# Kernel tuning notes

Hardware: AMD Instinct MI355X
Metric: run time of the kernel (lower is better)

Reference implementation:

```python
import jax, jax.numpy as jnp
import numpy as np

B, S, HID, NH = 8, 384, 512, 8
HD = HID // NH
SCALE = float(np.sqrt(HID))  # torch code scales by sqrt(full hidden_units), not head dim
EPS = 1e-6


def setup_inputs() -> dict:
    key = jax.random.key(0)
    ks = jax.random.split(key, 6)
    enc = jax.random.normal(ks[0], (B, S, HID), jnp.float32)
    # mask: (B,1,S,S); fill=ones, made causal (lower-triangular) so masking is exercised
    mask = jnp.broadcast_to(jnp.tril(jnp.ones((S, S), jnp.int32)), (B, 1, S, S))
    init = 1.0 / np.sqrt(HID)
    Wq = jax.random.normal(ks[1], (HID, HID), jnp.float32) * init
    Wk = jax.random.normal(ks[2], (HID, HID), jnp.float32) * init
    Wv = jax.random.normal(ks[3], (HID, HID), jnp.float32) * init
    Wo = jax.random.normal(ks[4], (HID, HID), jnp.float32) * init
    ln_gamma = jnp.ones((HID,), jnp.float32)
    ln_beta = jnp.zeros((HID,), jnp.float32)
    return {"enc": enc, "mask": mask, "Wq": Wq, "Wk": Wk, "Wv": Wv, "Wo": Wo,
            "ln_gamma": ln_gamma, "ln_beta": ln_beta}


def reference(enc, mask, Wq, Wk, Wv, Wo, ln_gamma, ln_beta):
    # enc: (B,S,HID); torch Linear(no bias): y = x @ W.T
    def heads(x, W):
        return (x @ W.T).reshape(B, S, NH, HD).transpose(0, 2, 1, 3)  # (B,H,S,D)

    q, k, v = heads(enc, Wq), heads(enc, Wk), heads(enc, Wv)
    # intersample scores: query (b,h,q) vs key (c,h,k) -> (B,H,C,Sq,Sk)
    scores = jnp.einsum('bhqd,chkd->bhcqk', q, k) / SCALE
    m = mask[:, 0]  # (C,S,S): key-sample mask
    scores = jnp.where(m[None, None] == 0, -1.0e9, scores)
    # joint softmax over (key-sample c, key-position k)
    sw = scores.transpose(0, 1, 3, 2, 4).reshape(B, NH, S, B * S)
    w = jax.nn.softmax(sw, axis=-1).reshape(B, NH, S, B, S).transpose(0, 1, 3, 2, 4)  # (B,H,C,Sq,Sk)
    ctx = jnp.einsum('bhcqk,chkd->bhqd', w, v)            # (B,H,S,D)
    ctx = ctx.transpose(0, 2, 1, 3).reshape(B, S, HID)     # (B,S,HID)
    out = ctx @ Wo.T + enc                                 # W_O + residual (dropout=identity, eval)
    mu = out.mean(-1, keepdims=True)
    var = ((out - mu) ** 2).mean(-1, keepdims=True)
    out = (out - mu) / jnp.sqrt(var + EPS) * ln_gamma + ln_beta
    return (out, w)
```

## Files before the change

### kernel.cpp

```cpp
#include <hip/hip_runtime.h>
#include <hip/hip_cooperative_groups.h>
#include <hip/hip_bf16.h>

namespace cg = cooperative_groups;

#define B_    8
#define S_    384
#define HID_  512
#define NH_   8
#define HD_   64
#define T_    3072
static constexpr float INV_SCALE = 0.044194173824159216f;

typedef float  f32x4  __attribute__((ext_vector_type(4)));
typedef __bf16 bf16x8 __attribute__((ext_vector_type(8)));
typedef __bf16 bf16x4 __attribute__((ext_vector_type(4)));

#define MFMA(a, b, c) __builtin_amdgcn_mfma_f32_16x16x32_bf16((a), (b), (c), 0, 0, 0)

#define NTHR 512
#define SMEM_BYTES 22528


__device__ __forceinline__ void cvt_unit(int i,
    const float* __restrict__ enc, const float* __restrict__ Wq,
    const float* __restrict__ Wk,  const float* __restrict__ Wv,
    const float* __restrict__ Wo,
    __bf16* __restrict__ encB, __bf16* __restrict__ WqB,
    __bf16* __restrict__ WkB,  __bf16* __restrict__ WvB,
    __bf16* __restrict__ WoB)
{
    const int E  = T_ * HID_ / 4;
    const int W4 = HID_ * HID_ / 4;
    const float* src; __bf16* dst; int off;
    if      (i < E)          { src = enc; dst = encB; off = i; }
    else if (i < E + W4)     { src = Wq;  dst = WqB;  off = i - E; }
    else if (i < E + 2 * W4) { src = Wk;  dst = WkB;  off = i - E - W4; }
    else if (i < E + 3 * W4) { src = Wv;  dst = WvB;  off = i - E - 2 * W4; }
    else                     { src = Wo;  dst = WoB;  off = i - E - 3 * W4; }
    f32x4 v = *(const f32x4*)(src + (size_t)off * 4);
    bf16x4 o;
    #pragma unroll
    for (int j = 0; j < 4; ++j) o[j] = (__bf16)v[j];
    *(bf16x4*)(dst + (size_t)off * 4) = o;
}

__device__ __forceinline__ void qkv_unit(int vb, int t2,
    const __bf16* __restrict__ encB, const __bf16* __restrict__ WqB,
    const __bf16* __restrict__ WkB,  const __bf16* __restrict__ WvB,
    __bf16* __restrict__ Qs, __bf16* __restrict__ Ks, __bf16* __restrict__ Vt)
{
    const int w    = t2 >> 6;
    const int lane = t2 & 63;
    const int col  = lane & 15;
    const int quad = lane >> 4;
    const int x  = vb % 48;
    const int y  = (vb / 48) % 8;
    const int z  = vb / 384;
    const int m0 = x * 64 + w * 16;
    const int n0 = y * 64;
    const __bf16* W = (z == 0) ? WqB : (z == 1) ? WkB : WvB;

    f32x4 acc[4];
    #pragma unroll
    for (int j = 0; j < 4; ++j) acc[j] = (f32x4){0.f, 0.f, 0.f, 0.f};

    const __bf16* arow = encB + (size_t)(m0 + col) * HID_;
    for (int k0 = 0; k0 < HID_; k0 += 32) {
        bf16x8 a = *(const bf16x8*)(arow + k0 + quad * 8);
        #pragma unroll
        for (int j = 0; j < 4; ++j) {
            bf16x8 b = *(const bf16x8*)(W + (size_t)(n0 + j * 16 + col) * HID_ + k0 + quad * 8);
            acc[j] = MFMA(a, b, acc[j]);
        }
    }

    if (z == 2) {
        #pragma unroll
        for (int j = 0; j < 4; ++j) {
            int n = n0 + j * 16 + col;
            bf16x4 pk;
            #pragma unroll
            for (int r = 0; r < 4; ++r) pk[r] = (__bf16)acc[j][r];
            *(bf16x4*)(Vt + (size_t)n * T_ + m0 + quad * 4) = pk;
        }
    } else {
        __bf16* Oo = (z == 0) ? Qs : Ks;
        float sc = (z == 0) ? INV_SCALE : 1.0f;
        #pragma unroll
        for (int j = 0; j < 4; ++j)
            #pragma unroll
            for (int r = 0; r < 4; ++r)
                Oo[(size_t)(m0 + quad * 4 + r) * HID_ + n0 + j * 16 + col] =
                    (__bf16)(acc[j][r] * sc);
    }
}

__device__ __forceinline__ void attn_unit(int qt, int h, int b, int tid, char* smem,
    const __bf16* __restrict__ Qs, const __bf16* __restrict__ Ks,
    const __bf16* __restrict__ Vt, __bf16* __restrict__ ctxB,
    float* __restrict__ rlws, __bf16* __restrict__ eB,
    float* __restrict__ wout, int useBf16)
{
    const int W    = tid >> 6;
    const int half = W >> 2;
    const int w    = W & 3;
    const int lane = tid & 63;
    const int col  = lane & 15;
    const int quad = lane >> 4;

    __bf16 (*elds)[16][72] = (__bf16(*)[16][72])(smem);
    float  (*cred)[16][68] = (float(*)[16][68])(smem);
    float  (*lred)[16][16] = (float(*)[16][16])(smem + 18432);

    const int qq_base = w * 16 + quad * 4;

    const __bf16* qrow = Qs + (size_t)(b * S_ + qt * 64 + w * 16 + col) * HID_ + h * HD_;
    bf16x8 aQ0 = *(const bf16x8*)(qrow + quad * 8);
    bf16x8 aQ1 = *(const bf16x8*)(qrow + 32 + quad * 8);

    f32x4 acc[4];
    #pragma unroll
    for (int j = 0; j < 4; ++j) acc[j] = (f32x4){0.f, 0.f, 0.f, 0.f};
    float lp[4] = {0.f, 0.f, 0.f, 0.f};

    const size_t qg   = (size_t)(b * NH_ + h) * S_ + qt * 64 + w * 16 + col;
    __bf16* ebase = eB + qg * T_;
    float*  wbase = wout + (((size_t)(b * NH_ + h) * B_) * S_ + qt * 64 + w * 16 + col) * S_;

    const int NC = B_ * (qt + 1);
    for (int idx = half; idx < NC; idx += 2) {
        const int c  = idx / (qt + 1);
        const int kc = idx % (qt + 1);
        const int kt0 = c * S_ + kc * 64;
        const bool diag = (kc == qt);
        #pragma unroll
        for (int nt = 0; nt < 4; ++nt) {
            const __bf16* krow = Ks + (size_t)(kt0 + nt * 16 + col) * HID_ + h * HD_;
            bf16x8 bK0 = *(const bf16x8*)(krow + quad * 8);
            bf16x8 bK1 = *(const bf16x8*)(krow + 32 + quad * 8);
            f32x4 s = (f32x4){0.f, 0.f, 0.f, 0.f};
            s = MFMA(aQ0, bK0, s);
            s = MFMA(aQ1, bK1, s);
            const int kk = nt * 16 + col;
            #pragma unroll
            for (int r = 0; r < 4; ++r) {
                float e = (!diag || kk <= qq_base + r) ? __expf(s[r]) : 0.f;
                lp[r] += e;
                elds[W][quad * 4 + r][kk] = (__bf16)e;
            }
        }
        #pragma unroll
        for (int ks = 0; ks < 2; ++ks) {
            bf16x8 aE = *(const bf16x8*)(&elds[W][col][ks * 32 + quad * 8]);
            if (useBf16) {
                *(bf16x8*)(ebase + c * S_ + kc * 64 + ks * 32 + quad * 8) = aE;
            } else {
                float* wp = wbase + (size_t)c * S_ * S_ + kc * 64 + ks * 32 + quad * 8;
                f32x4 lo, hi;
                #pragma unroll
                for (int j = 0; j < 4; ++j) { lo[j] = (float)aE[j]; hi[j] = (float)aE[j + 4]; }
                *(f32x4*)wp = lo;
                *(f32x4*)(wp + 4) = hi;
            }
            #pragma unroll
            for (int nt = 0; nt < 4; ++nt) {
                bf16x8 bV = *(const bf16x8*)(Vt + (size_t)(h * HD_ + nt * 16 + col) * T_ +
                                             kt0 + ks * 32 + quad * 8);
                acc[nt] = MFMA(aE, bV, acc[nt]);
            }
        }
    }

    __syncthreads();

    if (half == 1) {
        #pragma unroll
        for (int nt = 0; nt < 4; ++nt)
            #pragma unroll
            for (int r = 0; r < 4; ++r)
                cred[w][quad * 4 + r][nt * 16 + col] = acc[nt][r];
        #pragma unroll
        for (int r = 0; r < 4; ++r)
            lred[w][quad * 4 + r][col] = lp[r];
    }
    __syncthreads();
    if (half == 0) {
        #pragma unroll
        for (int r = 0; r < 4; ++r)
            lp[r] += lred[w][quad * 4 + r][col];
        #pragma unroll
        for (int nt = 0; nt < 4; ++nt)
            #pragma unroll
            for (int r = 0; r < 4; ++r)
                acc[nt][r] += cred[w][quad * 4 + r][nt * 16 + col];

        float rl[4];
        #pragma unroll
        for (int r = 0; r < 4; ++r) {
            float v = lp[r];
            v += __shfl_xor(v, 1);
            v += __shfl_xor(v, 2);
            v += __shfl_xor(v, 4);
            v += __shfl_xor(v, 8);
            rl[r] = 1.0f / v;
        }
        if (col == 0) {
            #pragma unroll
            for (int r = 0; r < 4; ++r)
                rlws[(size_t)(b * NH_ + h) * S_ + qt * 64 + qq_base + r] = rl[r];
        }
        #pragma unroll
        for (int nt = 0; nt < 4; ++nt)
            #pragma unroll
            for (int r = 0; r < 4; ++r)
                ctxB[(size_t)(b * S_ + qt * 64 + qq_base + r) * HID_ + h * HD_ + nt * 16 + col] =
                    (__bf16)(acc[nt][r] * rl[r]);
    }
}

__device__ __forceinline__ void wscale_unit(int u2, int tid, int nthr,
    const float* __restrict__ rlws, const __bf16* __restrict__ eB,
    float* __restrict__ wout, int useBf16)
{
    const int bh = u2 >> 3;
    const int c  = u2 & 7;
    float* wbase = wout + ((size_t)bh * B_ + c) * S_ * S_;
    const __bf16* ebase = eB + (size_t)bh * S_ * T_ + c * S_;
    const float* rlbase = rlws + (size_t)bh * S_;

    const int NCHUNK = S_ * (S_ / 8);
    for (int idx = tid; idx < NCHUNK; idx += nthr) {
        const int q  = idx / 48;
        const int k8 = (idx - q * 48) * 8;
        float* wp = wbase + (size_t)q * S_ + k8;
        if ((k8 >> 6) > (q >> 6)) {
            *(f32x4*)wp       = (f32x4){0.f, 0.f, 0.f, 0.f};
            *(f32x4*)(wp + 4) = (f32x4){0.f, 0.f, 0.f, 0.f};
        } else {
            const float rl = rlbase[q];
            f32x4 lo, hi;
            if (useBf16) {
                bf16x8 e = *(const bf16x8*)(ebase + (size_t)q * T_ + k8);
                #pragma unroll
                for (int j = 0; j < 4; ++j) { lo[j] = (float)e[j] * rl; hi[j] = (float)e[j + 4] * rl; }
            } else {
                f32x4 e0 = *(const f32x4*)wp;
                f32x4 e1 = *(const f32x4*)(wp + 4);
                #pragma unroll
                for (int j = 0; j < 4; ++j) { lo[j] = e0[j] * rl; hi[j] = e1[j] * rl; }
            }
            *(f32x4*)wp       = lo;
            *(f32x4*)(wp + 4) = hi;
        }
    }
}

__global__ __launch_bounds__(512, 2)
void mega2(const float* __restrict__ enc,
           const float* __restrict__ Wq,  const float* __restrict__ Wk,
           const float* __restrict__ Wv,  const float* __restrict__ Wo,
           const float* __restrict__ gamma, const float* __restrict__ beta,
           __bf16* __restrict__ encB, __bf16* __restrict__ WqB,
           __bf16* __restrict__ WkB,  __bf16* __restrict__ WvB,
           __bf16* __restrict__ WoB,
           __bf16* __restrict__ Qs,   __bf16* __restrict__ Ks,
           __bf16* __restrict__ Vt,   __bf16* __restrict__ ctxB,
           float* __restrict__ rlws,  __bf16* __restrict__ eB,
           float* __restrict__ wout,  float* __restrict__ out, int useBf16)
{
    cg::grid_group grid = cg::this_grid();
    const int blk  = blockIdx.x;
    const int nblk = gridDim.x;
    const int tid  = threadIdx.x;

    __shared__ __align__(16) char smem[SMEM_BYTES];

    {
        const int TOT = T_ * HID_ / 4 + HID_ * HID_;
        for (int i = blk * NTHR + tid; i < TOT; i += nblk * NTHR)
            cvt_unit(i, enc, Wq, Wk, Wv, Wo, encB, WqB, WkB, WvB, WoB);
    }
    grid.sync();

    {
        const int half = tid >> 8;
        const int t2   = tid & 255;
        for (int u = blk; u < 576; u += nblk)
            qkv_unit(u * 2 + half, t2, encB, WqB, WkB, WvB, Qs, Ks, Vt);
    }
    grid.sync();

    for (int i = blk; i < 384; i += nblk) {
        const int qt = 5 - (i >> 6);
        const int r  = i & 63;
        attn_unit(qt, r & 7, r >> 3, tid, smem, Qs, Ks, Vt, ctxB, rlws, eB, wout, useBf16);
        __syncthreads();
    }
    grid.sync();

    for (int u = blk; u < 704; u += nblk) {
        if (u < 192) {
            const int t0   = u * 16;
            const int wv   = tid >> 6;
            const int lane = tid & 63;
            const int col  = lane & 15;
            const int quad = lane >> 4;
            float (*s_sums)[8][2] = (float(*)[8][2])(smem);

            f32x4 acc[4];
            #pragma unroll
            for (int nt = 0; nt < 4; ++nt) acc[nt] = (f32x4){0.f, 0.f, 0.f, 0.f};

            const __bf16* arow = ctxB + (size_t)(t0 + col) * HID_;
            for (int step = 0; step < 16; ++step) {
                bf16x8 a = *(const bf16x8*)(arow + step * 32 + quad * 8);
                #pragma unroll
                for (int nt = 0; nt < 4; ++nt) {
                    bf16x8 bW = *(const bf16x8*)(WoB + (size_t)(wv * 64 + nt * 16 + col) * HID_ +
                                                 step * 32 + quad * 8);
                    acc[nt] = MFMA(a, bW, acc[nt]);
                }
            }

            const int trow = t0 + quad * 4;
            float psum[4] = {0.f, 0.f, 0.f, 0.f};
            float psq[4]  = {0.f, 0.f, 0.f, 0.f};
            #pragma unroll
            for (int nt = 0; nt < 4; ++nt) {
                int n = wv * 64 + nt * 16 + col;
                #pragma unroll
                for (int r = 0; r < 4; ++r) {
                    float x = acc[nt][r] + enc[(size_t)(trow + r) * HID_ + n];
                    acc[nt][r] = x;
                    psum[r] += x;
                    psq[r]  += x * x;
                }
            }
            #pragma unroll
            for (int r = 0; r < 4; ++r) {
                float v = psum[r], q2 = psq[r];
                v  += __shfl_xor(v, 1);  v  += __shfl_xor(v, 2);
                v  += __shfl_xor(v, 4);  v  += __shfl_xor(v, 8);
                q2 += __shfl_xor(q2, 1); q2 += __shfl_xor(q2, 2);
                q2 += __shfl_xor(q2, 4); q2 += __shfl_xor(q2, 8);
                if (col == 0) {
                    s_sums[quad * 4 + r][wv][0] = v;
                    s_sums[quad * 4 + r][wv][1] = q2;
                }
            }
            __syncthreads();

            #pragma unroll
            for (int r = 0; r < 4; ++r) {
                float sm = 0.f, sq = 0.f;
                #pragma unroll
                for (int q = 0; q < 8; ++q) {
                    sm += s_sums[quad * 4 + r][q][0];
                    sq += s_sums[quad * 4 + r][q][1];
                }
                float mu   = sm * (1.0f / 512.0f);
                float var  = sq * (1.0f / 512.0f) - mu * mu;
                float rstd = rsqrtf(var + 1e-6f);
                #pragma unroll
                for (int nt = 0; nt < 4; ++nt) {
                    int n = wv * 64 + nt * 16 + col;
                    float y = (acc[nt][r] - mu) * rstd * gamma[n] + beta[n];
                    out[(size_t)(trow + r) * HID_ + n] = y;
                }
            }
            __syncthreads();
        } else {
            wscale_unit(u - 192, tid, NTHR, rlws, eB, wout, useBf16);
        }
    }
}

__global__ __launch_bounds__(256)
void cvt_kernel(const float* enc, const float* Wq, const float* Wk,
                const float* Wv, const float* Wo,
                __bf16* encB, __bf16* WqB, __bf16* WkB, __bf16* WvB, __bf16* WoB)
{
    int i = blockIdx.x * 256 + threadIdx.x;
    cvt_unit(i, enc, Wq, Wk, Wv, Wo, encB, WqB, WkB, WvB, WoB);
}

__global__ __launch_bounds__(256)
void qkv_kernel(const __bf16* encB, const __bf16* WqB, const __bf16* WkB,
                const __bf16* WvB, __bf16* Qs, __bf16* Ks, __bf16* Vt)
{
    int vb = blockIdx.x + 48 * (blockIdx.y + 8 * blockIdx.z);
    qkv_unit(vb, threadIdx.x, encB, WqB, WkB, WvB, Qs, Ks, Vt);
}

__global__ __launch_bounds__(512)
void attn_sep(const __bf16* Qs, const __bf16* Ks, const __bf16* Vt,
              __bf16* ctxB, float* rlws, __bf16* eB, float* wout, int useBf16)
{
    __shared__ __align__(16) char smem[SMEM_BYTES];
    const int i  = blockIdx.x;
    const int qt = 5 - (i >> 6);
    const int r  = i & 63;
    attn_unit(qt, r & 7, r >> 3, threadIdx.x, smem, Qs, Ks, Vt, ctxB, rlws, eB, wout, useBf16);
}

__global__ __launch_bounds__(256)
void tail2(const float* __restrict__ rlws, const __bf16* __restrict__ eB,
           const __bf16* __restrict__ ctxB, const __bf16* __restrict__ WoB,
           const float* __restrict__ enc, const float* __restrict__ gamma,
           const float* __restrict__ beta, float* __restrict__ wout,
           float* __restrict__ out, int useBf16)
{
    const int tid = threadIdx.x;

    if (blockIdx.x < 192) {
        const int w    = tid >> 6;
        const int lane = tid & 63;
        const int col  = lane & 15;
        const int quad = lane >> 4;
        __shared__ float s_sums[16][4][2];

        const int t0 = blockIdx.x * 16;
        const int wv = w;

        f32x4 acc[8];
        #pragma unroll
        for (int nt = 0; nt < 8; ++nt) acc[nt] = (f32x4){0.f, 0.f, 0.f, 0.f};

        const __bf16* arow = ctxB + (size_t)(t0 + col) * HID_;
        for (int step = 0; step < 16; ++step) {
            bf16x8 a = *(const bf16x8*)(arow + step * 32 + quad * 8);
            #pragma unroll
            for (int nt = 0; nt < 8; ++nt) {
                bf16x8 bW = *(const bf16x8*)(WoB + (size_t)(wv * 128 + nt * 16 + col) * HID_ +
                                             step * 32 + quad * 8);
                acc[nt] = MFMA(a, bW, acc[nt]);
            }
        }

        const int trow = t0 + quad * 4;
        float psum[4] = {0.f, 0.f, 0.f, 0.f};
        float psq[4]  = {0.f, 0.f, 0.f, 0.f};
        #pragma unroll
        for (int nt = 0; nt < 8; ++nt) {
            int n = wv * 128 + nt * 16 + col;
            #pragma unroll
            for (int r = 0; r < 4; ++r) {
                float x = acc[nt][r] + enc[(size_t)(trow + r) * HID_ + n];
                acc[nt][r] = x;
                psum[r] += x;
                psq[r]  += x * x;
            }
        }
        #pragma unroll
        for (int r = 0; r < 4; ++r) {
            float v = psum[r], q2 = psq[r];
            v  += __shfl_xor(v, 1);  v  += __shfl_xor(v, 2);
            v  += __shfl_xor(v, 4);  v  += __shfl_xor(v, 8);
            q2 += __shfl_xor(q2, 1); q2 += __shfl_xor(q2, 2);
            q2 += __shfl_xor(q2, 4); q2 += __shfl_xor(q2, 8);
            if (col == 0) {
                s_sums[quad * 4 + r][wv][0] = v;
                s_sums[quad * 4 + r][wv][1] = q2;
            }
        }
        __syncthreads();

        #pragma unroll
        for (int r = 0; r < 4; ++r) {
            float sm = s_sums[quad * 4 + r][0][0] + s_sums[quad * 4 + r][1][0] +
                       s_sums[quad * 4 + r][2][0] + s_sums[quad * 4 + r][3][0];
            float sq = s_sums[quad * 4 + r][0][1] + s_sums[quad * 4 + r][1][1] +
                       s_sums[quad * 4 + r][2][1] + s_sums[quad * 4 + r][3][1];
            float mu   = sm * (1.0f / 512.0f);
            float var  = sq * (1.0f / 512.0f) - mu * mu;
            float rstd = rsqrtf(var + 1e-6f);
            #pragma unroll
            for (int nt = 0; nt < 8; ++nt) {
                int n = wv * 128 + nt * 16 + col;
                float y = (acc[nt][r] - mu) * rstd * gamma[n] + beta[n];
                out[(size_t)(trow + r) * HID_ + n] = y;
            }
        }
        return;
    }

    wscale_unit(blockIdx.x - 192, tid, 256, rlws, eB, wout, useBf16);
}

extern "C" void kernel_launch(void* const* d_in, const int* in_sizes, int n_in,
                              void* d_out, int out_size, void* d_ws, size_t ws_size,
                              hipStream_t stream)
{
    const float* enc   = (const float*)d_in[0];
    const float* Wq    = (const float*)d_in[2];
    const float* Wk    = (const float*)d_in[3];
    const float* Wv    = (const float*)d_in[4];
    const float* Wo    = (const float*)d_in[5];
    const float* gamma = (const float*)d_in[6];
    const float* beta  = (const float*)d_in[7];

    float* out  = (float*)d_out;
    float* wout = out + (size_t)T_ * HID_;

    char* ws = (char*)d_ws;
    const size_t SZ_TOK = (size_t)T_ * HID_ * sizeof(__bf16);
    const size_t SZ_W   = (size_t)HID_ * HID_ * sizeof(__bf16);
    __bf16* encB = (__bf16*)(ws);
    __bf16* WqB  = (__bf16*)(ws + SZ_TOK);
    __bf16* WkB  = (__bf16*)(ws + SZ_TOK + SZ_W);
    __bf16* WvB  = (__bf16*)(ws + SZ_TOK + 2 * SZ_W);
    __bf16* WoB  = (__bf16*)(ws + SZ_TOK + 3 * SZ_W);
    __bf16* Qs   = (__bf16*)(ws + SZ_TOK + 4 * SZ_W);
    __bf16* Ks   = (__bf16*)(ws + 2 * SZ_TOK + 4 * SZ_W);
    __bf16* Vt   = (__bf16*)(ws + 3 * SZ_TOK + 4 * SZ_W);
    __bf16* ctxB = (__bf16*)(ws + 4 * SZ_TOK + 4 * SZ_W);
    float*  rlws = (float*)(ws);

    const size_t BASE   = 5 * SZ_TOK + 4 * SZ_W;
    const size_t SZ_EB  = (size_t)(B_ * NH_) * S_ * T_ * sizeof(__bf16);
    int useBf16 = (ws_size >= BASE + SZ_EB) ? 1 : 0;
    __bf16* eB = (__bf16*)(ws + BASE);

    static int coop_ok = -1;
    static int nblk = 256;
    if (coop_ok < 0) {
        int dev = 0;
        (void)hipGetDevice(&dev);
        int attr = 0;
        (void)hipDeviceGetAttribute(&attr, hipDeviceAttributeCooperativeLaunch, dev);
        int occ = 0;
        (void)hipOccupancyMaxActiveBlocksPerMultiprocessor(&occ, mega2, NTHR, 0);
        int nCU = 0;
        (void)hipDeviceGetAttribute(&nCU, hipDeviceAttributeMultiprocessorCount, dev);
        coop_ok = (attr != 0 && occ >= 1) ? 1 : 0;
        long g = (long)occ * (long)nCU;
        if (g < 256)  g = 256;
        if (g > 1024) g = 1024;
        nblk = (int)g;
    }

    bool done = false;
    if (coop_ok == 1) {
        void* args[] = {
            (void*)&enc, (void*)&Wq, (void*)&Wk, (void*)&Wv, (void*)&Wo,
            (void*)&gamma, (void*)&beta,
            (void*)&encB, (void*)&WqB, (void*)&WkB, (void*)&WvB, (void*)&WoB,
            (void*)&Qs, (void*)&Ks, (void*)&Vt, (void*)&ctxB,
            (void*)&rlws, (void*)&eB, (void*)&wout, (void*)&out, (void*)&useBf16
        };
        hipError_t e = hipLaunchCooperativeKernel((void*)mega2, dim3(nblk),
                                                  dim3(NTHR), args, 0, stream);
        if (e != hipSuccess && nblk > 256) {
            nblk = 256;
            e = hipLaunchCooperativeKernel((void*)mega2, dim3(nblk),
                                           dim3(NTHR), args, 0, stream);
        }
        if (e == hipSuccess) done = true;
        else coop_ok = 0;
    }
    if (!done) {
        cvt_kernel<<<dim3(2560), 256, 0, stream>>>(enc, Wq, Wk, Wv, Wo,
                                                   encB, WqB, WkB, WvB, WoB);
        qkv_kernel<<<dim3(48, 8, 3), 256, 0, stream>>>(encB, WqB, WkB, WvB, Qs, Ks, Vt);
        attn_sep<<<dim3(384), 512, 0, stream>>>(Qs, Ks, Vt, ctxB, rlws, eB, wout, useBf16);
        tail2<<<dim3(192 + 512), 256, 0, stream>>>(rlws, eB, ctxB, WoB, enc,
                                                   gamma, beta, wout, out, useBf16);
    }
}
```

Baseline: 558.9 us.

## Fuse attention-weight normalization into attention unit, drop separate wscale phase

Each attention work unit now rescales its own unnormalized exp scores into the output weight tensor right after computing the row reciprocal sums, using a shared-memory copy of the reciprocals. The separate wscale pass in the final phase is removed, so that phase only runs the output projection plus layernorm. The goal is to overlap the large weight-tensor writes with attention work, avoid a second read of the reciprocal sums from global memory, and shorten the last grid-synced phase. The grid size is now fixed at 512 blocks instead of being derived from occupancy, which risks a cooperative launch failure or imbalance if fewer blocks fit; attention units that were already imbalanced (causal qt sizes) now carry extra rescale work.

```diff
diff --git a/kernel.cpp b/kernel.cpp
--- a/kernel.cpp
+++ b/kernel.cpp
@@ -19,7 +19,7 @@
 #define MFMA(a, b, c) __builtin_amdgcn_mfma_f32_16x16x32_bf16((a), (b), (c), 0, 0, 0)
 
 #define NTHR 512
-#define SMEM_BYTES 22528
+#define SMEM_BYTES 22784
 
 
 __device__ __forceinline__ void cvt_unit(int i,
@@ -112,6 +112,7 @@
     __bf16 (*elds)[16][72] = (__bf16(*)[16][72])(smem);
     float  (*cred)[16][68] = (float(*)[16][68])(smem);
     float  (*lred)[16][16] = (float(*)[16][16])(smem + 18432);
+    float*  rlsh           = (float*)(smem + 22528);
 
     const int qq_base = w * 16 + quad * 4;
 
@@ -124,9 +125,9 @@
     for (int j = 0; j < 4; ++j) acc[j] = (f32x4){0.f, 0.f, 0.f, 0.f};
     float lp[4] = {0.f, 0.f, 0.f, 0.f};
 
-    const size_t qg   = (size_t)(b * NH_ + h) * S_ + qt * 64 + w * 16 + col;
-    __bf16* ebase = eB + qg * T_;
-    float*  wbase = wout + (((size_t)(b * NH_ + h) * B_) * S_ + qt * 64 + w * 16 + col) * S_;
+    const size_t bh = (size_t)(b * NH_ + h);
+    __bf16* ebase = eB + (bh * S_ + qt * 64 + w * 16 + col) * T_;
+    float*  wbase = wout + ((bh * B_) * S_ + qt * 64 + w * 16 + col) * S_;
 
     const int NC = B_ * (qt + 1);
     for (int idx = half; idx < NC; idx += 2) {
@@ -207,8 +208,10 @@
         }
         if (col == 0) {
             #pragma unroll
-            for (int r = 0; r < 4; ++r)
-                rlws[(size_t)(b * NH_ + h) * S_ + qt * 64 + qq_base + r] = rl[r];
+            for (int r = 0; r < 4; ++r) {
+                rlws[bh * S_ + qt * 64 + qq_base + r] = rl[r];
+                rlsh[qq_base + r] = rl[r];
+            }
         }
         #pragma unroll
         for (int nt = 0; nt < 4; ++nt)
@@ -217,31 +220,25 @@
                 ctxB[(size_t)(b * S_ + qt * 64 + qq_base + r) * HID_ + h * HD_ + nt * 16 + col] =
                     (__bf16)(acc[nt][r] * rl[r]);
     }
-}
-
-__device__ __forceinline__ void wscale_unit(int u2, int tid, int nthr,
-    const float* __restrict__ rlws, const __bf16* __restrict__ eB,
-    float* __restrict__ wout, int useBf16)
-{
-    const int bh = u2 >> 3;
-    const int c  = u2 & 7;
-    float* wbase = wout + ((size_t)bh * B_ + c) * S_ * S_;
-    const __bf16* ebase = eB + (size_t)bh * S_ * T_ + c * S_;
-    const float* rlbase = rlws + (size_t)bh * S_;
-
-    const int NCHUNK = S_ * (S_ / 8);
-    for (int idx = tid; idx < NCHUNK; idx += nthr) {
-        const int q  = idx / 48;
-        const int k8 = (idx - q * 48) * 8;
-        float* wp = wbase + (size_t)q * S_ + k8;
-        if ((k8 >> 6) > (q >> 6)) {
+    __syncthreads();
+
+    const __bf16* eunit = eB + (bh * S_ + qt * 64) * T_;
+    float* wunit = wout + (bh * B_) * S_ * S_;
+    for (int g = tid; g < 24576; g += NTHR) {
+        const int k8   = g % 48;
+        const int rest = g / 48;
+        const int ql   = rest & 63;
+        const int c    = rest >> 6;
+        const int k    = k8 * 8;
+        float* wp = wunit + ((size_t)c * S_ + qt * 64 + ql) * S_ + k;
+        if ((k >> 6) > qt) {
             *(f32x4*)wp       = (f32x4){0.f, 0.f, 0.f, 0.f};
             *(f32x4*)(wp + 4) = (f32x4){0.f, 0.f, 0.f, 0.f};
         } else {
-            const float rl = rlbase[q];
+            const float rl = rlsh[ql];
             f32x4 lo, hi;
             if (useBf16) {
-                bf16x8 e = *(const bf16x8*)(ebase + (size_t)q * T_ + k8);
+                bf16x8 e = *(const bf16x8*)(eunit + (size_t)ql * T_ + c * S_ + k);
                 #pragma unroll
                 for (int j = 0; j < 4; ++j) { lo[j] = (float)e[j] * rl; hi[j] = (float)e[j + 4] * rl; }
             } else {
@@ -299,140 +296,24 @@
     }
     grid.sync();
 
-    for (int u = blk; u < 704; u += nblk) {
-        if (u < 192) {
-            const int t0   = u * 16;
-            const int wv   = tid >> 6;
-            const int lane = tid & 63;
-            const int col  = lane & 15;
-            const int quad = lane >> 4;
-            float (*s_sums)[8][2] = (float(*)[8][2])(smem);
-
-            f32x4 acc[4];
-            #pragma unroll
-            for (int nt = 0; nt < 4; ++nt) acc[nt] = (f32x4){0.f, 0.f, 0.f, 0.f};
-
-            const __bf16* arow = ctxB + (size_t)(t0 + col) * HID_;
-            for (int step = 0; step < 16; ++step) {
-                bf16x8 a = *(const bf16x8*)(arow + step * 32 + quad * 8);
-                #pragma unroll
-                for (int nt = 0; nt < 4; ++nt) {
-                    bf16x8 bW = *(const bf16x8*)(WoB + (size_t)(wv * 64 + nt * 16 + col) * HID_ +
-                                                 step * 32 + quad * 8);
-                    acc[nt] = MFMA(a, bW, acc[nt]);
-                }
-            }
-
-            const int trow = t0 + quad * 4;
-            float psum[4] = {0.f, 0.f, 0.f, 0.f};
-            float psq[4]  = {0.f, 0.f, 0.f, 0.f};
-            #pragma unroll
-            for (int nt = 0; nt < 4; ++nt) {
-                int n = wv * 64 + nt * 16 + col;
-                #pragma unroll
-                for (int r = 0; r < 4; ++r) {
-                    float x = acc[nt][r] + enc[(size_t)(trow + r) * HID_ + n];
-                    acc[nt][r] = x;
-                    psum[r] += x;
-                    psq[r]  += x * x;
-                }
-            }
-            #pragma unroll
-            for (int r = 0; r < 4; ++r) {
-                float v = psum[r], q2 = psq[r];
-                v  += __shfl_xor(v, 1);  v  += __shfl_xor(v, 2);
-                v  += __shfl_xor(v, 4);  v  += __shfl_xor(v, 8);
-                q2 += __shfl_xor(q2, 1); q2 += __shfl_xor(q2, 2);
-                q2 += __shfl_xor(q2, 4); q2 += __shfl_xor(q2, 8);
-                if (col == 0) {
-                    s_sums[quad * 4 + r][wv][0] = v;
-                    s_sums[quad * 4 + r][wv][1] = q2;
-                }
-            }
-            __syncthreads();
-
-            #pragma unroll
-            for (int r = 0; r < 4; ++r) {
-                float sm = 0.f, sq = 0.f;
-                #pragma unroll
-                for (int q = 0; q < 8; ++q) {
-                    sm += s_sums[quad * 4 + r][q][0];
-                    sq += s_sums[quad * 4 + r][q][1];
-                }
-                float mu   = sm * (1.0f / 512.0f);
-                float var  = sq * (1.0f / 512.0f) - mu * mu;
-                float rstd = rsqrtf(var + 1e-6f);
-                #pragma unroll
-                for (int nt = 0; nt < 4; ++nt) {
-                    int n = wv * 64 + nt * 16 + col;
-                    float y = (acc[nt][r] - mu) * rstd * gamma[n] + beta[n];
-                    out[(size_t)(trow + r) * HID_ + n] = y;
-                }
-            }
-            __syncthreads();
-        } else {
-            wscale_unit(u - 192, tid, NTHR, rlws, eB, wout, useBf16);
-        }
-    }
-}
-
-__global__ __launch_bounds__(256)
-void cvt_kernel(const float* enc, const float* Wq, const float* Wk,
-                const float* Wv, const float* Wo,
-                __bf16* encB, __bf16* WqB, __bf16* WkB, __bf16* WvB, __bf16* WoB)
-{
-    int i = blockIdx.x * 256 + threadIdx.x;
-    cvt_unit(i, enc, Wq, Wk, Wv, Wo, encB, WqB, WkB, WvB, WoB);
-}
-
-__global__ __launch_bounds__(256)
-void qkv_kernel(const __bf16* encB, const __bf16* WqB, const __bf16* WkB,
-                const __bf16* WvB, __bf16* Qs, __bf16* Ks, __bf16* Vt)
-{
-    int vb = blockIdx.x + 48 * (blockIdx.y + 8 * blockIdx.z);
-    qkv_unit(vb, threadIdx.x, encB, WqB, WkB, WvB, Qs, Ks, Vt);
-}
-
-__global__ __launch_bounds__(512)
-void attn_sep(const __bf16* Qs, const __bf16* Ks, const __bf16* Vt,
-              __bf16* ctxB, float* rlws, __bf16* eB, float* wout, int useBf16)
-{
-    __shared__ __align__(16) char smem[SMEM_BYTES];
-    const int i  = blockIdx.x;
-    const int qt = 5 - (i >> 6);
-    const int r  = i & 63;
-    attn_unit(qt, r & 7, r >> 3, threadIdx.x, smem, Qs, Ks, Vt, ctxB, rlws, eB, wout, useBf16);
-}
-
-__global__ __launch_bounds__(256)
-void tail2(const float* __restrict__ rlws, const __bf16* __restrict__ eB,
-           const __bf16* __restrict__ ctxB, const __bf16* __restrict__ WoB,
-           const float* __restrict__ enc, const float* __restrict__ gamma,
-           const float* __restrict__ beta, float* __restrict__ wout,
-           float* __restrict__ out, int useBf16)
-{
-    const int tid = threadIdx.x;
-
-    if (blockIdx.x < 192) {
-        const int w    = tid >> 6;
+    for (int u = blk; u < 192; u += nblk) {
+        const int t0   = u * 16;
+        const int wv   = tid >> 6;
         const int lane = tid & 63;
         const int col  = lane & 15;
         const int quad = lane >> 4;
-        __shared__ float s_sums[16][4][2];
-
-        const int t0 = blockIdx.x * 16;
-        const int wv = w;
-
-        f32x4 acc[8];
-        #pragma unroll
-        for (int nt = 0; nt < 8; ++nt) acc[nt] = (f32x4){0.f, 0.f, 0.f, 0.f};
+        float (*s_sums)[8][2] = (float(*)[8][2])(smem);
+
+        f32x4 acc[4];
+        #pragma unroll
+        for (int nt = 0; nt < 4; ++nt) acc[nt] = (f32x4){0.f, 0.f, 0.f, 0.f};
 
         const __bf16* arow = ctxB + (size_t)(t0 + col) * HID_;
         for (int step = 0; step < 16; ++step) {
             bf16x8 a = *(const bf16x8*)(arow + step * 32 + quad * 8);
             #pragma unroll
-            for (int nt = 0; nt < 8; ++nt) {
-                bf16x8 bW = *(const bf16x8*)(WoB + (size_t)(wv * 128 + nt * 16 + col) * HID_ +
+            for (int nt = 0; nt < 4; ++nt) {
+                bf16x8 bW = *(const bf16x8*)(WoB + (size_t)(wv * 64 + nt * 16 + col) * HID_ +
                                              step * 32 + quad * 8);
                 acc[nt] = MFMA(a, bW, acc[nt]);
             }
@@ -442,8 +323,8 @@
         float psum[4] = {0.f, 0.f, 0.f, 0.f};
         float psq[4]  = {0.f, 0.f, 0.f, 0.f};
         #pragma unroll
-        for (int nt = 0; nt < 8; ++nt) {
-            int n = wv * 128 + nt * 16 + col;
+        for (int nt = 0; nt < 4; ++nt) {
+            int n = wv * 64 + nt * 16 + col;
             #pragma unroll
             for (int r = 0; r < 4; ++r) {
                 float x = acc[nt][r] + enc[(size_t)(trow + r) * HID_ + n];
@@ -468,24 +349,128 @@
 
         #pragma unroll
         for (int r = 0; r < 4; ++r) {
-            float sm = s_sums[quad * 4 + r][0][0] + s_sums[quad * 4 + r][1][0] +
-                       s_sums[quad * 4 + r][2][0] + s_sums[quad * 4 + r][3][0];
-            float sq = s_sums[quad * 4 + r][0][1] + s_sums[quad * 4 + r][1][1] +
-                       s_sums[quad * 4 + r][2][1] + s_sums[quad * 4 + r][3][1];
+            float sm = 0.f, sq = 0.f;
+            #pragma unroll
+            for (int q = 0; q < 8; ++q) {
+                sm += s_sums[quad * 4 + r][q][0];
+                sq += s_sums[quad * 4 + r][q][1];
+            }
             float mu   = sm * (1.0f / 512.0f);
             float var  = sq * (1.0f / 512.0f) - mu * mu;
             float rstd = rsqrtf(var + 1e-6f);
             #pragma unroll
-            for (int nt = 0; nt < 8; ++nt) {
-                int n = wv * 128 + nt * 16 + col;
+            for (int nt = 0; nt < 4; ++nt) {
+                int n = wv * 64 + nt * 16 + col;
                 float y = (acc[nt][r] - mu) * rstd * gamma[n] + beta[n];
                 out[(size_t)(trow + r) * HID_ + n] = y;
             }
         }
-        return;
-    }
-
-    wscale_unit(blockIdx.x - 192, tid, 256, rlws, eB, wout, useBf16);
+        __syncthreads();
+    }
+}
+
+__global__ __launch_bounds__(256)
+void cvt_kernel(const float* enc, const float* Wq, const float* Wk,
+                const float* Wv, const float* Wo,
+                __bf16* encB, __bf16* WqB, __bf16* WkB, __bf16* WvB, __bf16* WoB)
+{
+    int i = blockIdx.x * 256 + threadIdx.x;
+    cvt_unit(i, enc, Wq, Wk, Wv, Wo, encB, WqB, WkB, WvB, WoB);
+}
+
+__global__ __launch_bounds__(256)
+void qkv_kernel(const __bf16* encB, const __bf16* WqB, const __bf16* WkB,
+                const __bf16* WvB, __bf16* Qs, __bf16* Ks, __bf16* Vt)
+{
+    int vb = blockIdx.x + 48 * (blockIdx.y + 8 * blockIdx.z);
+    qkv_unit(vb, threadIdx.x, encB, WqB, WkB, WvB, Qs, Ks, Vt);
+}
+
+__global__ __launch_bounds__(512)
+void attn_sep(const __bf16* Qs, const __bf16* Ks, const __bf16* Vt,
+              __bf16* ctxB, float* rlws, __bf16* eB, float* wout, int useBf16)
+{
+    __shared__ __align__(16) char smem[SMEM_BYTES];
+    const int i  = blockIdx.x;
+    const int qt = 5 - (i >> 6);
+    const int r  = i & 63;
+    attn_unit(qt, r & 7, r >> 3, threadIdx.x, smem, Qs, Ks, Vt, ctxB, rlws, eB, wout, useBf16);
+}
+
+__global__ __launch_bounds__(256)
+void tail2(const __bf16* __restrict__ ctxB, const __bf16* __restrict__ WoB,
+           const float* __restrict__ enc, const float* __restrict__ gamma,
+           const float* __restrict__ beta, float* __restrict__ out)
+{
+    const int tid  = threadIdx.x;
+    const int w    = tid >> 6;
+    const int lane = tid & 63;
+    const int col  = lane & 15;
+    const int quad = lane >> 4;
+    __shared__ float s_sums[16][4][2];
+
+    const int t0 = blockIdx.x * 16;
+    const int wv = w;
+
+    f32x4 acc[8];
+    #pragma unroll
+    for (int nt = 0; nt < 8; ++nt) acc[nt] = (f32x4){0.f, 0.f, 0.f, 0.f};
+
+    const __bf16* arow = ctxB + (size_t)(t0 + col) * HID_;
+    for (int step = 0; step < 16; ++step) {
+        bf16x8 a = *(const bf16x8*)(arow + step * 32 + quad * 8);
+        #pragma unroll
+        for (int nt = 0; nt < 8; ++nt) {
+            bf16x8 bW = *(const bf16x8*)(WoB + (size_t)(wv * 128 + nt * 16 + col) * HID_ +
+                                         step * 32 + quad * 8);
+            acc[nt] = MFMA(a, bW, acc[nt]);
+        }
+    }
+
+    const int trow = t0 + quad * 4;
+    float psum[4] = {0.f, 0.f, 0.f, 0.f};
+    float psq[4]  = {0.f, 0.f, 0.f, 0.f};
+    #pragma unroll
+    for (int nt = 0; nt < 8; ++nt) {
+        int n = wv * 128 + nt * 16 + col;
+        #pragma unroll
+        for (int r = 0; r < 4; ++r) {
+            float x = acc[nt][r] + enc[(size_t)(trow + r) * HID_ + n];
+            acc[nt][r] = x;
+            psum[r] += x;
+            psq[r]  += x * x;
+        }
+    }
+    #pragma unroll
+    for (int r = 0; r < 4; ++r) {
+        float v = psum[r], q2 = psq[r];
+        v  += __shfl_xor(v, 1);  v  += __shfl_xor(v, 2);
+        v  += __shfl_xor(v, 4);  v  += __shfl_xor(v, 8);
+        q2 += __shfl_xor(q2, 1); q2 += __shfl_xor(q2, 2);
+        q2 += __shfl_xor(q2, 4); q2 += __shfl_xor(q2, 8);
+        if (col == 0) {
+            s_sums[quad * 4 + r][wv][0] = v;
+            s_sums[quad * 4 + r][wv][1] = q2;
+        }
+    }
+    __syncthreads();
+
+    #pragma unroll
+    for (int r = 0; r < 4; ++r) {
+        float sm = s_sums[quad * 4 + r][0][0] + s_sums[quad * 4 + r][1][0] +
+                   s_sums[quad * 4 + r][2][0] + s_sums[quad * 4 + r][3][0];
+        float sq = s_sums[quad * 4 + r][0][1] + s_sums[quad * 4 + r][1][1] +
+                   s_sums[quad * 4 + r][2][1] + s_sums[quad * 4 + r][3][1];
+        float mu   = sm * (1.0f / 512.0f);
+        float var  = sq * (1.0f / 512.0f) - mu * mu;
+        float rstd = rsqrtf(var + 1e-6f);
+        #pragma unroll
+        for (int nt = 0; nt < 8; ++nt) {
+            int n = wv * 128 + nt * 16 + col;
+            float y = (acc[nt][r] - mu) * rstd * gamma[n] + beta[n];
+            out[(size_t)(trow + r) * HID_ + n] = y;
+        }
+    }
 }
 
 extern "C" void kernel_launch(void* const* d_in, const int* in_sizes, int n_in,
@@ -523,21 +508,13 @@
     __bf16* eB = (__bf16*)(ws + BASE);
 
     static int coop_ok = -1;
-    static int nblk = 256;
+    static int nblk = 512;
     if (coop_ok < 0) {
         int dev = 0;
         (void)hipGetDevice(&dev);
         int attr = 0;
         (void)hipDeviceGetAttribute(&attr, hipDeviceAttributeCooperativeLaunch, dev);
-        int occ = 0;
-        (void)hipOccupancyMaxActiveBlocksPerMultiprocessor(&occ, mega2, NTHR, 0);
-        int nCU = 0;
-        (void)hipDeviceGetAttribute(&nCU, hipDeviceAttributeMultiprocessorCount, dev);
-        coop_ok = (attr != 0 && occ >= 1) ? 1 : 0;
-        long g = (long)occ * (long)nCU;
-        if (g < 256)  g = 256;
-        if (g > 1024) g = 1024;
-        nblk = (int)g;
+        coop_ok = (attr != 0) ? 1 : 0;
     }
 
     bool done = false;
@@ -564,7 +541,6 @@
                                                    encB, WqB, WkB, WvB, WoB);
         qkv_kernel<<<dim3(48, 8, 3), 256, 0, stream>>>(encB, WqB, WkB, WvB, Qs, Ks, Vt);
         attn_sep<<<dim3(384), 512, 0, stream>>>(Qs, Ks, Vt, ctxB, rlws, eB, wout, useBf16);
-        tail2<<<dim3(192 + 512), 256, 0, stream>>>(rlws, eB, ctxB, WoB, enc,
-                                                   gamma, beta, wout, out, useBf16);
-    }
-}
+        tail2<<<dim3(192), 256, 0, stream>>>(ctxB, WoB, enc, gamma, beta, out);
+    }
+}
```

Result: slower. 668.3 us (+19.6%).
